# Kernel tuning notes

Measured on AMD Instinct MI355X. Metric: run time of the kernel, lower is better.

The kernel has to match this reference:

```python
import jax, jax.numpy as jnp
import numpy as np


def setup_inputs() -> dict:
    key = jax.random.key(0)
    ks = jax.random.split(key, 8)
    T, B, NIN, NHID, NOUT = 512, 128, 64, 1024, 10
    # parameter scales mirror the torch init: input weights std 0.01, recurrent std 0.005
    return {
        "u": jax.random.normal(ks[0], (T, B, NIN), jnp.float32),
        "W_uz": jax.random.normal(ks[1], (NIN, NHID), jnp.float32) * 0.01,
        "W_hz": jax.random.normal(ks[2], (NHID, NHID), jnp.float32) * 0.005,
        "b_z": jnp.full((NHID,), -2.0, jnp.float32),
        "W_ur": jax.random.normal(ks[3], (NIN, NHID), jnp.float32) * 0.01,
        "W_hr": jax.random.normal(ks[4], (NHID, NHID), jnp.float32) * 0.005,
        "b_r": jnp.zeros((NHID,), jnp.float32),
        "W_uh": jax.random.normal(ks[5], (NIN, NHID), jnp.float32) * 0.01,
        "W_hh": jax.random.normal(ks[6], (NHID, NHID), jnp.float32) * 0.01,
        "b_h": jnp.zeros((NHID,), jnp.float32),
        "W_hy": jax.random.normal(ks[7], (NHID, NOUT), jnp.float32) * 0.01,
        "b_y": jnp.zeros((NOUT,), jnp.float32),
    }


def reference(u, W_uz, W_hz, b_z, W_ur, W_hr, b_r, W_uh, W_hh, b_h, W_hy, b_y):
    T, B, _ = u.shape
    nhid = W_hh.shape[0]
    # Precompute input projections for all timesteps (one big GEMM each):
    # (T,B,nin) @ (nin,nhid) -> (T,B,nhid)
    uz = jnp.einsum("tbi,ih->tbh", u, W_uz) + b_z
    ur = jnp.einsum("tbi,ih->tbh", u, W_ur) + b_r
    uh = jnp.einsum("tbi,ih->tbh", u, W_uh) + b_h

    def step(h, xs):
        xz, xr, xh = xs
        z = jax.nn.sigmoid(xz + h @ W_hz)          # update gate (B,nhid)
        r = jax.nn.sigmoid(xr + h @ W_hr)          # reset gate
        h_tilde = jnp.tanh(xh + (r * h) @ W_hh)    # candidate
        h_new = (1.0 - z) * h + z * h_tilde
        return h_new, None

    h0 = jnp.zeros((B, nhid), u.dtype)
    h_final, _ = jax.lax.scan(step, h0, (uz, ur, uh))
    logits = h_final @ W_hy + b_y                  # (B,nout), 'lastSoftmax'
    return logits, h_final
```

## Files before the change

### kernel.cpp

```cpp
#include <hip/hip_runtime.h>

#define NHID 1024
#define NB   128
#define NIN  64
#define TSTEPS 512
#define NBLK 256
#define NTHR 512
#define GROW 8
#define SLOTN (NB * NHID)

typedef __attribute__((ext_vector_type(8))) short short8v;
typedef __attribute__((ext_vector_type(4))) float f32x4;
typedef __attribute__((ext_vector_type(4))) unsigned u32x4;

__device__ __forceinline__ short8v ld8(const unsigned short* p) {
  return *reinterpret_cast<const short8v*>(p);
}

__device__ __forceinline__ unsigned short f2b(float x) {
  union { float f; unsigned u; } v; v.f = x;
  unsigned r = v.u + 0x7fffu + ((v.u >> 16) & 1u);
  return (unsigned short)(r >> 16);
}

__device__ __forceinline__ void cstore16(unsigned short* p, unsigned short v) {
  __hip_atomic_store(p, v, __ATOMIC_RELAXED, __HIP_MEMORY_SCOPE_AGENT);
}

__device__ __forceinline__ bool ok16(u32x4 v) {
  unsigned bad = 0;
#pragma unroll
  for (int i = 0; i < 4; ++i) {
    bad |= (unsigned)((v[i] & 0xFFFFu) == 0xFFFFu);
    bad |= (unsigned)((v[i] >> 16) == 0xFFFFu);
  }
  return bad == 0;
}

struct GruParams {
  const unsigned short* u;
  const unsigned short* WhzT; const unsigned short* WhrT; const unsigned short* WhhT;
  const unsigned short* WuzT; const unsigned short* WurT; const unsigned short* WuhT;
  const float* bz; const float* br; const float* bh;
  float* h;
  unsigned short* hb;
  unsigned short* sb;
};

__global__ __launch_bounds__(NTHR, 2) void gru_main(GruParams p) {
  __shared__ unsigned short stage[GROW * NHID];
  __shared__ float red[2][4][4][64];

  const int tid  = threadIdx.x;
  const int lane = tid & 63;
  const int w    = tid >> 6;
  const int ct   = w & 3;
  const int kh   = w >> 2;
  const int rg   = blockIdx.x >> 4;
  const int cg   = blockIdx.x & 15;
  const int lr   = lane & 15;
  const int ar_  = lr & 7;
  const int lk   = (lane >> 4) * 8;

  const int colN = cg * 64 + ct * 16 + lr;
  const unsigned short* wz  = p.WhzT + (size_t)colN * NHID + kh * 512 + lk;
  const unsigned short* wr  = p.WhrT + (size_t)colN * NHID + kh * 512 + lk;
  const unsigned short* wh  = p.WhhT + (size_t)colN * NHID + kh * 512 + lk;
  const unsigned short* wuz = p.WuzT + colN * NIN + lk;
  const unsigned short* wur = p.WurT + colN * NIN + lk;
  const unsigned short* wuh = p.WuhT + colN * NIN + lk;

  const int orow0 = (lane >> 4) * 4;
  const bool owner = orow0 < GROW;
  const float bzv = p.bz[colN];
  const float brv = p.br[colN];
  const float bhv = p.bh[colN];

  const u32x4 poisonv = {0xFFFFFFFFu, 0xFFFFFFFFu, 0xFFFFFFFFu, 0xFFFFFFFFu};

  short8v Wz[16], Wr[16], Wh[16];
#pragma unroll
  for (int it = 0; it < 16; ++it) {
    Wz[it] = ld8(wz + it * 32);
    Wr[it] = ld8(wr + it * 32);
    Wh[it] = ld8(wh + it * 32);
  }

  float h_own[4] = {0.f, 0.f, 0.f, 0.f};
  float zreg[4];

#define PSTAGE(SRC)                                                              \
  {                                                                              \
    int j0 = tid, j1 = tid + NTHR;                                               \
    const void* g0 = (SRC) + (j0 >> 7) * NHID + (j0 & 127) * 8;                  \
    const void* g1 = (SRC) + (j1 >> 7) * NHID + (j1 & 127) * 8;                  \
    char* d0 = (char*)stage +                                                    \
               (((j0 >> 7) * 2048) | (((j0 & 127) * 16) ^ (((j0 >> 7) & 7) << 4)));\
    char* d1 = (char*)stage +                                                    \
               (((j1 >> 7) * 2048) | (((j1 & 127) * 16) ^ (((j1 >> 7) & 7) << 4)));\
    u32x4 v0 = poisonv, v1 = poisonv;                                            \
    bool k0 = false, k1 = false;                                                 \
    for (int spin = 0; spin < (1 << 13); ++spin) {                               \
      if (!k0) asm volatile("global_load_dwordx4 %0, %1, off sc0 sc1"            \
                            : "=v"(v0) : "v"(g0) : "memory");                    \
      if (!k1) asm volatile("global_load_dwordx4 %0, %1, off sc0 sc1"            \
                            : "=v"(v1) : "v"(g1) : "memory");                    \
      asm volatile("s_waitcnt vmcnt(0)" ::: "memory");                           \
      k0 = k0 || ok16(v0);                                                       \
      k1 = k1 || ok16(v1);                                                       \
      if (k0 && k1) break;                                                       \
    }                                                                            \
    *(u32x4*)d0 = v0;                                                            \
    *(u32x4*)d1 = v1;                                                            \
  }

#define REPOISON(SLOTSLICE)                                                      \
  if (tid < 64) {                                                                \
    void* rp = (SLOTSLICE) + (tid >> 3) * NHID + cg * 64 + (tid & 7) * 8;        \
    asm volatile("global_store_dwordx4 %0, %1, off sc0 sc1"                      \
                 :: "v"(rp), "v"(poisonv) : "memory");                           \
  }

#define LDSA(IT)                                                                \
  (*(const short8v*)((const char*)stage +                                       \
     ((ar_ * 2048) | ((((kh * 512 + (IT) * 32 + lk) * 2)) ^ (ar_ << 4)))))

  for (int t = 0; t < TSTEPS; ++t) {
    const int sA = t & 3;
    const int sP = (t + 3) & 3;
    const int sW = (t + 1) & 3;
    const unsigned short* au = p.u + ((size_t)t * NB + rg * GROW + ar_) * NIN + lk;

    f32x4 az = {0.f, 0.f, 0.f, 0.f};
    f32x4 ar = {0.f, 0.f, 0.f, 0.f};
    if (kh) {
#pragma unroll
      for (int it = 0; it < 2; ++it) {
        short8v a = ld8(au + it * 32);
        az = __builtin_amdgcn_mfma_f32_16x16x32_bf16(a, ld8(wuz + it * 32), az, 0, 0, 0);
        ar = __builtin_amdgcn_mfma_f32_16x16x32_bf16(a, ld8(wur + it * 32), ar, 0, 0, 0);
      }
    }
    PSTAGE(p.hb + sA * SLOTN + rg * GROW * NHID);
    REPOISON(p.sb + sP * SLOTN + rg * GROW * NHID);
    asm volatile("s_waitcnt vmcnt(0)" ::: "memory");
    __syncthreads();

#pragma unroll
    for (int it = 0; it < 16; ++it) {
      short8v a = LDSA(it);
      az = __builtin_amdgcn_mfma_f32_16x16x32_bf16(a, Wz[it], az, 0, 0, 0);
      ar = __builtin_amdgcn_mfma_f32_16x16x32_bf16(a, Wr[it], ar, 0, 0, 0);
    }
    if (kh) {
#pragma unroll
      for (int j = 0; j < 4; ++j) { red[0][ct][j][lane] = az[j]; red[1][ct][j][lane] = ar[j]; }
    }
    __syncthreads();
    if (!kh && owner) {
#pragma unroll
      for (int i = 0; i < 4; ++i) {
        float z = 1.f / (1.f + __expf(-(az[i] + red[0][ct][i][lane] + bzv)));
        float r = 1.f / (1.f + __expf(-(ar[i] + red[1][ct][i][lane] + brv)));
        zreg[i] = z;
        cstore16(p.sb + sA * SLOTN + (size_t)(rg * GROW + orow0 + i) * NHID + colN,
                 f2b(r * h_own[i]));
      }
    }

    f32x4 ac = {0.f, 0.f, 0.f, 0.f};
    if (kh) {
#pragma unroll
      for (int it = 0; it < 2; ++it) {
        ac = __builtin_amdgcn_mfma_f32_16x16x32_bf16(ld8(au + it * 32), ld8(wuh + it * 32), ac, 0, 0, 0);
      }
    }
    PSTAGE(p.sb + sA * SLOTN + rg * GROW * NHID);
    REPOISON(p.hb + sP * SLOTN + rg * GROW * NHID);
    asm volatile("s_waitcnt vmcnt(0)" ::: "memory");
    __syncthreads();

#pragma unroll
    for (int it = 0; it < 16; ++it) {
      ac = __builtin_amdgcn_mfma_f32_16x16x32_bf16(LDSA(it), Wh[it], ac, 0, 0, 0);
    }
    if (kh) {
#pragma unroll
      for (int j = 0; j < 4; ++j) red[0][ct][j][lane] = ac[j];
    }
    __syncthreads();
    if (!kh && owner) {
#pragma unroll
      for (int i = 0; i < 4; ++i) {
        float x = ac[i] + red[0][ct][i][lane] + bhv;
        float e = __expf(2.f * x);
        float ht = 1.f - 2.f / (e + 1.f);
        float hn = (1.f - zreg[i]) * h_own[i] + zreg[i] * ht;
        h_own[i] = hn;
        cstore16(p.hb + sW * SLOTN + (size_t)(rg * GROW + orow0 + i) * NHID + colN, f2b(hn));
      }
      if (t == TSTEPS - 1) {
#pragma unroll
        for (int i = 0; i < 4; ++i)
          p.h[(size_t)(rg * GROW + orow0 + i) * NHID + colN] = h_own[i];
      }
    }
  }
#undef PSTAGE
#undef REPOISON
#undef LDSA
}

__global__ void k_transpose_bf16(const float* in, unsigned short* out, int R, int C) {
  int idx = blockIdx.x * 256 + threadIdx.x;
  if (idx < R * C) {
    int r = idx / C, c = idx % C;
    out[(size_t)c * R + r] = f2b(in[idx]);
  }
}

__global__ void k_convert_bf16(const float* in, unsigned short* out, int n) {
  for (int i = blockIdx.x * 256 + threadIdx.x; i < n; i += gridDim.x * 256)
    out[i] = f2b(in[i]);
}

__global__ void k_logits(const float* __restrict__ h, const float* __restrict__ Why,
                         const float* __restrict__ by, float* __restrict__ out) {
  int row = blockIdx.x;
  int lane = threadIdx.x;
  float acc[10];
#pragma unroll
  for (int j = 0; j < 10; ++j) acc[j] = 0.f;
  for (int k = lane; k < NHID; k += 64) {
    float hv = h[row * NHID + k];
#pragma unroll
    for (int j = 0; j < 10; ++j) acc[j] += hv * Why[k * 10 + j];
  }
#pragma unroll
  for (int j = 0; j < 10; ++j)
    for (int off = 32; off; off >>= 1) acc[j] += __shfl_down(acc[j], off);
  if (lane == 0) {
#pragma unroll
    for (int j = 0; j < 10; ++j) out[row * 10 + j] = acc[j] + by[j];
  }
}

extern "C" void kernel_launch(void* const* d_in, const int* in_sizes, int n_in,
                              void* d_out, int out_size, void* d_ws, size_t ws_size,
                              hipStream_t stream) {
  (void)in_sizes; (void)n_in; (void)out_size; (void)ws_size;
  const float* u   = (const float*)d_in[0];
  const float* Wuz = (const float*)d_in[1];
  const float* Whz = (const float*)d_in[2];
  const float* bz  = (const float*)d_in[3];
  const float* Wur = (const float*)d_in[4];
  const float* Whr = (const float*)d_in[5];
  const float* br  = (const float*)d_in[6];
  const float* Wuh = (const float*)d_in[7];
  const float* Whh = (const float*)d_in[8];
  const float* bh  = (const float*)d_in[9];
  const float* Why = (const float*)d_in[10];
  const float* by  = (const float*)d_in[11];

  char* ws = (char*)d_ws;
  size_t off = 0;
  auto alloc = [&](size_t bytes) { char* p = ws + off; off += (bytes + 255) & ~255ull; return p; };
  unsigned short* WhzT = (unsigned short*)alloc((size_t)NHID * NHID * 2);
  unsigned short* WhrT = (unsigned short*)alloc((size_t)NHID * NHID * 2);
  unsigned short* WhhT = (unsigned short*)alloc((size_t)NHID * NHID * 2);
  unsigned short* WuzT = (unsigned short*)alloc((size_t)NHID * NIN * 2);
  unsigned short* WurT = (unsigned short*)alloc((size_t)NHID * NIN * 2);
  unsigned short* WuhT = (unsigned short*)alloc((size_t)NHID * NIN * 2);
  unsigned short* ub   = (unsigned short*)alloc((size_t)TSTEPS * NB * NIN * 2);
  unsigned short* hb   = (unsigned short*)alloc(4ull * SLOTN * 2);
  unsigned short* sb   = (unsigned short*)alloc(4ull * SLOTN * 2);

  float* out = (float*)d_out;
  float* hf  = out + NB * 10;

  int n1 = NHID * NHID;
  hipLaunchKernelGGL(k_transpose_bf16, dim3((n1 + 255) / 256), dim3(256), 0, stream, Whz, WhzT, NHID, NHID);
  hipLaunchKernelGGL(k_transpose_bf16, dim3((n1 + 255) / 256), dim3(256), 0, stream, Whr, WhrT, NHID, NHID);
  hipLaunchKernelGGL(k_transpose_bf16, dim3((n1 + 255) / 256), dim3(256), 0, stream, Whh, WhhT, NHID, NHID);
  int n2 = NIN * NHID;
  hipLaunchKernelGGL(k_transpose_bf16, dim3((n2 + 255) / 256), dim3(256), 0, stream, Wuz, WuzT, NIN, NHID);
  hipLaunchKernelGGL(k_transpose_bf16, dim3((n2 + 255) / 256), dim3(256), 0, stream, Wur, WurT, NIN, NHID);
  hipLaunchKernelGGL(k_transpose_bf16, dim3((n2 + 255) / 256), dim3(256), 0, stream, Wuh, WuhT, NIN, NHID);
  int n3 = TSTEPS * NB * NIN;
  hipLaunchKernelGGL(k_convert_bf16, dim3(2048), dim3(256), 0, stream, u, ub, n3);
  hipMemsetAsync(hb, 0, (size_t)SLOTN * 2, stream);
  hipMemsetAsync(hb + SLOTN, 0xFF, 3ull * SLOTN * 2, stream);
  hipMemsetAsync(sb, 0xFF, 4ull * SLOTN * 2, stream);

  GruParams p;
  p.u = ub; p.WhzT = WhzT; p.WhrT = WhrT; p.WhhT = WhhT;
  p.WuzT = WuzT; p.WurT = WurT; p.WuhT = WuhT;
  p.bz = bz; p.br = br; p.bh = bh;
  p.h = hf; p.hb = hb; p.sb = sb;
  hipLaunchKernelGGL(gru_main, dim3(NBLK), dim3(NTHR), 0, stream, p);

  hipLaunchKernelGGL(k_logits, dim3(NB), dim3(64), 0, stream, hf, Why, by, out);
}
```

Before: 3.706 ms.

## Vectorize gate epilogue into one wave with packed 16-byte stores

Both K-halves now write their partial sums to a padded, reorganized LDS reduction buffer. A single wave (tid<64) then sums the partials for 8 rows x 64 columns, applies the gates and emits the bf16 results as packed dwordx4 stores, replacing the per-element 16-bit atomic stores. The vmcnt wait that followed the staging and repoison is deferred until just before the next barrier, and only that wave performs it, so the repoison stores can overlap the MFMA loop. This cuts store-instruction count and the latency of the cross-block handoff, but the gate math is now serialized on one wave and correctness depends on the deferred wait covering the repoison ordering.

Measured after the change: 5.280 ms. 1.42x slower.

```diff
diff --git a/kernel.cpp b/kernel.cpp
--- a/kernel.cpp
+++ b/kernel.cpp
@@ -23,8 +23,8 @@
   return (unsigned short)(r >> 16);
 }
 
-__device__ __forceinline__ void cstore16(unsigned short* p, unsigned short v) {
-  __hip_atomic_store(p, v, __ATOMIC_RELAXED, __HIP_MEMORY_SCOPE_AGENT);
+__device__ __forceinline__ unsigned pk2(float a, float b) {
+  return (unsigned)f2b(a) | ((unsigned)f2b(b) << 16);
 }
 
 __device__ __forceinline__ bool ok16(u32x4 v) {
@@ -49,7 +49,7 @@
 
 __global__ __launch_bounds__(NTHR, 2) void gru_main(GruParams p) {
   __shared__ unsigned short stage[GROW * NHID];
-  __shared__ float red[2][4][4][64];
+  __shared__ float red[2][2][4][4][68];
 
   const int tid  = threadIdx.x;
   const int lane = tid & 63;
@@ -70,13 +70,21 @@
   const unsigned short* wur = p.WurT + colN * NIN + lk;
   const unsigned short* wuh = p.WuhT + colN * NIN + lk;
 
-  const int orow0 = (lane >> 4) * 4;
-  const bool owner = orow0 < GROW;
-  const float bzv = p.bz[colN];
-  const float brv = p.br[colN];
-  const float bhv = p.bh[colN];
-
   const u32x4 poisonv = {0xFFFFFFFFu, 0xFFFFFFFFu, 0xFFFFFFFFu, 0xFFFFFFFFu};
+
+  const int grow_ = tid >> 3;
+  const int gcc_  = tid & 7;
+  const int gct_  = gcc_ >> 1;
+  const int glane0 = (((grow_ >> 2) & 1) << 4) | ((gcc_ & 1) << 3);
+  const int greg_ = grow_ & 3;
+  const int gcol0 = cg * 64 + gcc_ * 8;
+
+  f32x4 bz0 = *(const f32x4*)(p.bz + gcol0);
+  f32x4 bz1 = *(const f32x4*)(p.bz + gcol0 + 4);
+  f32x4 br0 = *(const f32x4*)(p.br + gcol0);
+  f32x4 br1 = *(const f32x4*)(p.br + gcol0 + 4);
+  f32x4 bh0 = *(const f32x4*)(p.bh + gcol0);
+  f32x4 bh1 = *(const f32x4*)(p.bh + gcol0 + 4);
 
   short8v Wz[16], Wr[16], Wh[16];
 #pragma unroll
@@ -86,8 +94,8 @@
     Wh[it] = ld8(wh + it * 32);
   }
 
-  float h_own[4] = {0.f, 0.f, 0.f, 0.f};
-  float zreg[4];
+  float h_own[8] = {0.f, 0.f, 0.f, 0.f, 0.f, 0.f, 0.f, 0.f};
+  float zreg[8];
 
 #define PSTAGE(SRC)                                                              \
   {                                                                              \
@@ -143,7 +151,6 @@
     }
     PSTAGE(p.hb + sA * SLOTN + rg * GROW * NHID);
     REPOISON(p.sb + sP * SLOTN + rg * GROW * NHID);
-    asm volatile("s_waitcnt vmcnt(0)" ::: "memory");
     __syncthreads();
 
 #pragma unroll
@@ -152,20 +159,39 @@
       az = __builtin_amdgcn_mfma_f32_16x16x32_bf16(a, Wz[it], az, 0, 0, 0);
       ar = __builtin_amdgcn_mfma_f32_16x16x32_bf16(a, Wr[it], ar, 0, 0, 0);
     }
-    if (kh) {
-#pragma unroll
-      for (int j = 0; j < 4; ++j) { red[0][ct][j][lane] = az[j]; red[1][ct][j][lane] = ar[j]; }
-    }
+#pragma unroll
+    for (int j = 0; j < 4; ++j) {
+      red[0][kh][j][ct][lane] = az[j];
+      red[1][kh][j][ct][lane] = ar[j];
+    }
+    if (tid < 64) asm volatile("s_waitcnt vmcnt(0)" ::: "memory");
     __syncthreads();
-    if (!kh && owner) {
-#pragma unroll
-      for (int i = 0; i < 4; ++i) {
-        float z = 1.f / (1.f + __expf(-(az[i] + red[0][ct][i][lane] + bzv)));
-        float r = 1.f / (1.f + __expf(-(ar[i] + red[1][ct][i][lane] + brv)));
-        zreg[i] = z;
-        cstore16(p.sb + sA * SLOTN + (size_t)(rg * GROW + orow0 + i) * NHID + colN,
-                 f2b(r * h_own[i]));
-      }
+
+    if (tid < 64) {
+      f32x4 zs0 = *(const f32x4*)&red[0][0][greg_][gct_][glane0]
+                + *(const f32x4*)&red[0][1][greg_][gct_][glane0];
+      f32x4 zs1 = *(const f32x4*)&red[0][0][greg_][gct_][glane0 + 4]
+                + *(const f32x4*)&red[0][1][greg_][gct_][glane0 + 4];
+      f32x4 rs0 = *(const f32x4*)&red[1][0][greg_][gct_][glane0]
+                + *(const f32x4*)&red[1][1][greg_][gct_][glane0];
+      f32x4 rs1 = *(const f32x4*)&red[1][0][greg_][gct_][glane0 + 4]
+                + *(const f32x4*)&red[1][1][greg_][gct_][glane0 + 4];
+      float s8[8];
+#pragma unroll
+      for (int c = 0; c < 8; ++c) {
+        float zsum = (c < 4 ? zs0[c] : zs1[c - 4]) + (c < 4 ? bz0[c] : bz1[c - 4]);
+        float rsum = (c < 4 ? rs0[c] : rs1[c - 4]) + (c < 4 ? br0[c] : br1[c - 4]);
+        float zz = 1.f / (1.f + __expf(-zsum));
+        float rr = 1.f / (1.f + __expf(-rsum));
+        zreg[c] = zz;
+        s8[c] = rr * h_own[c];
+      }
+      u32x4 sv;
+      sv[0] = pk2(s8[0], s8[1]); sv[1] = pk2(s8[2], s8[3]);
+      sv[2] = pk2(s8[4], s8[5]); sv[3] = pk2(s8[6], s8[7]);
+      void* dst = p.sb + sA * SLOTN + (size_t)(rg * GROW + grow_) * NHID + gcol0;
+      asm volatile("global_store_dwordx4 %0, %1, off sc0 sc1"
+                   :: "v"(dst), "v"(sv) : "memory");
     }
 
     f32x4 ac = {0.f, 0.f, 0.f, 0.f};
@@ -177,32 +203,39 @@
     }
     PSTAGE(p.sb + sA * SLOTN + rg * GROW * NHID);
     REPOISON(p.hb + sP * SLOTN + rg * GROW * NHID);
-    asm volatile("s_waitcnt vmcnt(0)" ::: "memory");
     __syncthreads();
 
 #pragma unroll
     for (int it = 0; it < 16; ++it) {
       ac = __builtin_amdgcn_mfma_f32_16x16x32_bf16(LDSA(it), Wh[it], ac, 0, 0, 0);
     }
-    if (kh) {
-#pragma unroll
-      for (int j = 0; j < 4; ++j) red[0][ct][j][lane] = ac[j];
-    }
+#pragma unroll
+    for (int j = 0; j < 4; ++j) red[0][kh][j][ct][lane] = ac[j];
+    if (tid < 64) asm volatile("s_waitcnt vmcnt(0)" ::: "memory");
     __syncthreads();
-    if (!kh && owner) {
-#pragma unroll
-      for (int i = 0; i < 4; ++i) {
-        float x = ac[i] + red[0][ct][i][lane] + bhv;
+
+    if (tid < 64) {
+      f32x4 hs0 = *(const f32x4*)&red[0][0][greg_][gct_][glane0]
+                + *(const f32x4*)&red[0][1][greg_][gct_][glane0];
+      f32x4 hs1 = *(const f32x4*)&red[0][0][greg_][gct_][glane0 + 4]
+                + *(const f32x4*)&red[0][1][greg_][gct_][glane0 + 4];
+#pragma unroll
+      for (int c = 0; c < 8; ++c) {
+        float x = (c < 4 ? hs0[c] : hs1[c - 4]) + (c < 4 ? bh0[c] : bh1[c - 4]);
         float e = __expf(2.f * x);
         float ht = 1.f - 2.f / (e + 1.f);
-        float hn = (1.f - zreg[i]) * h_own[i] + zreg[i] * ht;
-        h_own[i] = hn;
-        cstore16(p.hb + sW * SLOTN + (size_t)(rg * GROW + orow0 + i) * NHID + colN, f2b(hn));
-      }
+        h_own[c] = (1.f - zreg[c]) * h_own[c] + zreg[c] * ht;
+      }
+      u32x4 hv;
+      hv[0] = pk2(h_own[0], h_own[1]); hv[1] = pk2(h_own[2], h_own[3]);
+      hv[2] = pk2(h_own[4], h_own[5]); hv[3] = pk2(h_own[6], h_own[7]);
+      void* dst = p.hb + sW * SLOTN + (size_t)(rg * GROW + grow_) * NHID + gcol0;
+      asm volatile("global_store_dwordx4 %0, %1, off sc0 sc1"
+                   :: "v"(dst), "v"(hv) : "memory");
       if (t == TSTEPS - 1) {
-#pragma unroll
-        for (int i = 0; i < 4; ++i)
-          p.h[(size_t)(rg * GROW + orow0 + i) * NHID + colN] = h_own[i];
+        float* ho = p.h + (size_t)(rg * GROW + grow_) * NHID + gcol0;
+        *(f32x4*)ho = *(const f32x4*)&h_own[0];
+        *(f32x4*)(ho + 4) = *(const f32x4*)&h_own[4];
       }
     }
   }
```

## Transpose exchange slot layout to column-major and pack four bf16 per 64-bit store

Applied to the files above, without the earlier changes.

Changes the global h/rh exchange buffers from row-major (row, col) to column-interleaved (col, 8 rows) layout. Each owner thread now packs its four bf16 outputs into one 64-bit atomic exchange instead of four separate 16-bit atomic stores. Readers load contiguous 16-byte chunks and scatter them into the swizzled LDS tile with eight 2-byte stores each, and the repoison addressing is updated to match. The aim is fewer, wider global writes on the cross-block critical path, paid for with more LDS store instructions per staged chunk.

New measurement: 3.564 ms. 1.04x faster.

```diff
diff --git a/kernel.cpp b/kernel.cpp
--- a/kernel.cpp
+++ b/kernel.cpp
@@ -21,10 +21,6 @@
   union { float f; unsigned u; } v; v.f = x;
   unsigned r = v.u + 0x7fffu + ((v.u >> 16) & 1u);
   return (unsigned short)(r >> 16);
-}
-
-__device__ __forceinline__ void cstore16(unsigned short* p, unsigned short v) {
-  __hip_atomic_store(p, v, __ATOMIC_RELAXED, __HIP_MEMORY_SCOPE_AGENT);
 }
 
 __device__ __forceinline__ bool ok16(u32x4 v) {
@@ -92,12 +88,8 @@
 #define PSTAGE(SRC)                                                              \
   {                                                                              \
     int j0 = tid, j1 = tid + NTHR;                                               \
-    const void* g0 = (SRC) + (j0 >> 7) * NHID + (j0 & 127) * 8;                  \
-    const void* g1 = (SRC) + (j1 >> 7) * NHID + (j1 & 127) * 8;                  \
-    char* d0 = (char*)stage +                                                    \
-               (((j0 >> 7) * 2048) | (((j0 & 127) * 16) ^ (((j0 >> 7) & 7) << 4)));\
-    char* d1 = (char*)stage +                                                    \
-               (((j1 >> 7) * 2048) | (((j1 & 127) * 16) ^ (((j1 >> 7) & 7) << 4)));\
+    const unsigned short* g0 = (SRC) + j0 * 8;                                   \
+    const unsigned short* g1 = (SRC) + j1 * 8;                                   \
     u32x4 v0 = poisonv, v1 = poisonv;                                            \
     bool k0 = false, k1 = false;                                                 \
     for (int spin = 0; spin < (1 << 13); ++spin) {                               \
@@ -110,13 +102,18 @@
       k1 = k1 || ok16(v1);                                                       \
       if (k0 && k1) break;                                                       \
     }                                                                            \
-    *(u32x4*)d0 = v0;                                                            \
-    *(u32x4*)d1 = v1;                                                            \
+    _Pragma("unroll")                                                            \
+    for (int r = 0; r < 8; ++r) {                                                \
+      unsigned short a0 = (unsigned short)(v0[r >> 1] >> ((r & 1) * 16));        \
+      unsigned short a1 = (unsigned short)(v1[r >> 1] >> ((r & 1) * 16));        \
+      *(unsigned short*)((char*)stage + ((r * 2048) | ((j0 * 2) ^ (r << 4)))) = a0; \
+      *(unsigned short*)((char*)stage + ((r * 2048) | ((j1 * 2) ^ (r << 4)))) = a1; \
+    }                                                                            \
   }
 
 #define REPOISON(SLOTSLICE)                                                      \
   if (tid < 64) {                                                                \
-    void* rp = (SLOTSLICE) + (tid >> 3) * NHID + cg * 64 + (tid & 7) * 8;        \
+    void* rp = (char*)(SLOTSLICE) + cg * 1024 + tid * 16;                        \
     asm volatile("global_store_dwordx4 %0, %1, off sc0 sc1"                      \
                  :: "v"(rp), "v"(poisonv) : "memory");                           \
   }
@@ -130,6 +127,8 @@
     const int sP = (t + 3) & 3;
     const int sW = (t + 1) & 3;
     const unsigned short* au = p.u + ((size_t)t * NB + rg * GROW + ar_) * NIN + lk;
+    unsigned short* hbR = p.hb + (size_t)sA * SLOTN + rg * GROW * NHID;
+    unsigned short* sbR = p.sb + (size_t)sA * SLOTN + rg * GROW * NHID;
 
     f32x4 az = {0.f, 0.f, 0.f, 0.f};
     f32x4 ar = {0.f, 0.f, 0.f, 0.f};
@@ -141,8 +140,8 @@
         ar = __builtin_amdgcn_mfma_f32_16x16x32_bf16(a, ld8(wur + it * 32), ar, 0, 0, 0);
       }
     }
-    PSTAGE(p.hb + sA * SLOTN + rg * GROW * NHID);
-    REPOISON(p.sb + sP * SLOTN + rg * GROW * NHID);
+    PSTAGE(hbR);
+    REPOISON(p.sb + (size_t)sP * SLOTN + rg * GROW * NHID);
     asm volatile("s_waitcnt vmcnt(0)" ::: "memory");
     __syncthreads();
 
@@ -158,14 +157,16 @@
     }
     __syncthreads();
     if (!kh && owner) {
+      unsigned long long sd = 0;
 #pragma unroll
       for (int i = 0; i < 4; ++i) {
         float z = 1.f / (1.f + __expf(-(az[i] + red[0][ct][i][lane] + bzv)));
         float r = 1.f / (1.f + __expf(-(ar[i] + red[1][ct][i][lane] + brv)));
         zreg[i] = z;
-        cstore16(p.sb + sA * SLOTN + (size_t)(rg * GROW + orow0 + i) * NHID + colN,
-                 f2b(r * h_own[i]));
-      }
+        sd |= (unsigned long long)f2b(r * h_own[i]) << (16 * i);
+      }
+      (void)__hip_atomic_exchange((unsigned long long*)(sbR + colN * 8 + orow0),
+                                  sd, __ATOMIC_RELAXED, __HIP_MEMORY_SCOPE_AGENT);
     }
 
     f32x4 ac = {0.f, 0.f, 0.f, 0.f};
@@ -175,8 +176,8 @@
         ac = __builtin_amdgcn_mfma_f32_16x16x32_bf16(ld8(au + it * 32), ld8(wuh + it * 32), ac, 0, 0, 0);
       }
     }
-    PSTAGE(p.sb + sA * SLOTN + rg * GROW * NHID);
-    REPOISON(p.hb + sP * SLOTN + rg * GROW * NHID);
+    PSTAGE(sbR);
+    REPOISON(p.hb + (size_t)sP * SLOTN + rg * GROW * NHID);
     asm volatile("s_waitcnt vmcnt(0)" ::: "memory");
     __syncthreads();
 
@@ -190,6 +191,7 @@
     }
     __syncthreads();
     if (!kh && owner) {
+      unsigned long long hd = 0;
 #pragma unroll
       for (int i = 0; i < 4; ++i) {
         float x = ac[i] + red[0][ct][i][lane] + bhv;
@@ -197,8 +199,11 @@
         float ht = 1.f - 2.f / (e + 1.f);
         float hn = (1.f - zreg[i]) * h_own[i] + zreg[i] * ht;
         h_own[i] = hn;
-        cstore16(p.hb + sW * SLOTN + (size_t)(rg * GROW + orow0 + i) * NHID + colN, f2b(hn));
-      }
+        hd |= (unsigned long long)f2b(hn) << (16 * i);
+      }
+      unsigned short* hbW = p.hb + (size_t)sW * SLOTN + rg * GROW * NHID;
+      (void)__hip_atomic_exchange((unsigned long long*)(hbW + colN * 8 + orow0),
+                                  hd, __ATOMIC_RELAXED, __HIP_MEMORY_SCOPE_AGENT);
       if (t == TSTEPS - 1) {
 #pragma unroll
         for (int i = 0; i < 4; ++i)
```
